# Kernel tuning notes

Measured on AMD Instinct MI355X. Metric: run time of the kernel, lower is better.

Reference implementation:

```python
import jax, jax.numpy as jnp
import numpy as np

D_MODEL = 1024
N_HEADS = 16
D_K = D_MODEL // N_HEADS
THETA = 10000.0


def _rope(x, token_positions):
    # x: [b, h, s, d_k]; interleaved RoPE (pairs at even/odd positions)
    half = D_K // 2
    inv_freq = 1.0 / (THETA ** (2.0 * jnp.arange(half, dtype=jnp.float32) / D_K))  # [half]
    angles = token_positions.astype(jnp.float32)[:, None] * inv_freq[None, :]      # [s, half]
    sin, cos = jnp.sin(angles), jnp.cos(angles)
    x_even = x[..., 0::2]
    x_odd = x[..., 1::2]
    out_even = cos * x_even - sin * x_odd
    out_odd = sin * x_even + cos * x_odd
    # interleave back: [..., half, 2] -> [..., d_k]
    return jnp.stack((out_even, out_odd), axis=-1).reshape(x.shape)


def setup_inputs() -> dict:
    key = jax.random.key(0)
    kx, kq, kk, kv, ko = jax.random.split(key, 5)
    b, s = 4, 2048
    std = (2.0 / (D_MODEL + D_MODEL)) ** 0.5
    return {
        "x": jax.random.normal(kx, (b, s, D_MODEL), dtype=jnp.float32),
        "Wq": jax.random.normal(kq, (D_MODEL, D_MODEL), dtype=jnp.float32) * std,
        "Wk": jax.random.normal(kk, (D_MODEL, D_MODEL), dtype=jnp.float32) * std,
        "Wv": jax.random.normal(kv, (D_MODEL, D_MODEL), dtype=jnp.float32) * std,
        "Wo": jax.random.normal(ko, (D_MODEL, D_MODEL), dtype=jnp.float32) * std,
        "token_positions": jnp.arange(s, dtype=jnp.int32),
    }


def reference(x, Wq, Wk, Wv, Wo, token_positions):
    b, s, _ = x.shape
    split = lambda t: t.reshape(b, s, N_HEADS, D_K).transpose(0, 2, 1, 3)  # b h s d
    q = split(x @ Wq.T)
    k = split(x @ Wk.T)
    v = split(x @ Wv.T)
    q = _rope(q, token_positions)
    k = _rope(k, token_positions)
    scores = jnp.einsum("bhnd,bhmd->bhnm", q, k) / jnp.sqrt(jnp.float32(D_K))
    causal = jnp.tril(jnp.ones((s, s), dtype=bool))
    scores = jnp.where(causal, scores, -jnp.inf)
    attn = jax.nn.softmax(scores, axis=-1)
    out = jnp.einsum("bhnm,bhmd->bhnd", attn, v)
    out = out.transpose(0, 2, 1, 3).reshape(b, s, D_MODEL)
    return out @ Wo.T
```

## Files before the change

kernel.cpp:

```cpp
#include <hip/hip_runtime.h>
#include <stdint.h>

typedef __attribute__((ext_vector_type(8))) __bf16 bf16x8;
typedef __attribute__((ext_vector_type(4))) float f32x4;
typedef __attribute__((ext_vector_type(16))) float f32x16;
typedef __attribute__((ext_vector_type(8))) unsigned short ushort8;

__device__ __forceinline__ unsigned short f2bf(float f){
  union { float f; unsigned int i; } v; v.f = f;
  unsigned int r = v.i + 0x7fffu + ((v.i >> 16) & 1u);
  return (unsigned short)(r >> 16);
}
__device__ __forceinline__ void gload16(const void* g, void* l){
  __builtin_amdgcn_global_load_lds((__attribute__((address_space(1))) void*)(g),
                                   (__attribute__((address_space(3))) void*)(l),
                                   16, 0, 0);
}
__device__ __forceinline__ unsigned int cvtpk(float lo, float hi){
  unsigned int r;
  asm("v_cvt_pk_bf16_f32 %0, %1, %2" : "=v"(r) : "v"(lo), "v"(hi));
  return r;
}
__device__ __forceinline__ bf16x8 ldsw(const char* tile, int row, int colb){
  return *(const bf16x8*)(tile + row*128 + (colb ^ ((row & 7) << 4)));
}

#define SEQ   2048
#define DM    1024
#define NH    16
#define DK    64
#define BATCH 4
#define MTOT  (BATCH*SEQ)
#define NX    (MTOT*DM)
#define NW    (DM*DM)

#define QSCALE 0.18033688011112f

__global__ __launch_bounds__(256) void k_tables(const int* __restrict__ pos,
                                                float* __restrict__ tab)
{
  const int idx = blockIdx.x * 256 + threadIdx.x;
  const int s = idx >> 5, i = idx & 31;
  const float inv = __expf(-0.28782313662425575f * (float)i);
  const float a = (float)pos[s] * inv;
  tab[2*idx]   = cosf(a);
  tab[2*idx+1] = sinf(a);
}

__global__ __launch_bounds__(256) void k_convert(
    const float* __restrict__ x,  const float* __restrict__ wq,
    const float* __restrict__ wk, const float* __restrict__ wv,
    const float* __restrict__ wo,
    unsigned short* __restrict__ xb, unsigned short* __restrict__ wb)
{
  const int tid = blockIdx.x * 256 + threadIdx.x;
  const long long e = (long long)tid * 8;
  const float* src; unsigned short* dst;
  if (e < NX) { src = x + e; dst = xb + e; }
  else {
    long long j = e - NX;
    int seg = (int)(j >> 20);
    long long off = j & 1048575;
    src = (seg==0?wq:seg==1?wk:seg==2?wv:wo) + off;
    dst = wb + (size_t)seg*NW + off;
  }
  const float4 a = *(const float4*)src;
  const float4 b = *(const float4*)(src + 4);
  uint4 o;
  o.x = (unsigned int)f2bf(a.x) | ((unsigned int)f2bf(a.y) << 16);
  o.y = (unsigned int)f2bf(a.z) | ((unsigned int)f2bf(a.w) << 16);
  o.z = (unsigned int)f2bf(b.x) | ((unsigned int)f2bf(b.y) << 16);
  o.w = (unsigned int)f2bf(b.z) | ((unsigned int)f2bf(b.w) << 16);
  *(uint4*)dst = o;
}

#define BK 32
#define NTK (DM/BK)

template<int MODE>
__global__ __launch_bounds__(512, 3) void k_gemm(
    const unsigned short* __restrict__ A,
    const unsigned short* __restrict__ Wb,
    unsigned short* __restrict__ D0,
    unsigned short* __restrict__ D1,
    unsigned short* __restrict__ D2,
    float* __restrict__ Dout,
    const float* __restrict__ tab)
{
  __shared__ __attribute__((aligned(16))) unsigned short As[2][256*BK];
  __shared__ __attribute__((aligned(16))) unsigned short Bs[2][128*BK];
  const int tid  = threadIdx.x;
  const int lane = tid & 63;
  const int w    = tid >> 6;
  const int wm = w >> 1, wn = w & 1;

  const int bid = blockIdx.x;
  const int tq  = bid >> 3;
  const int m0  = ((bid & 7)*4 + (tq & 3)) * 256;
  const int r   = tq >> 2;
  const int n0  = (MODE == 0 ? (r & 7) : r) * 128;
  const int z   = (MODE == 0) ? (r >> 3) : 0;

  const unsigned short* W = Wb + (size_t)z * NW;
  unsigned short* Dh = (MODE == 0) ? ((z == 0) ? D0 : (z == 1) ? D1 : D2) : nullptr;
  const bool vtr = (MODE == 0) && (z == 2);

  f32x4 acc[4][4];
  #pragma unroll
  for (int i = 0; i < 4; ++i)
    #pragma unroll
    for (int j = 0; j < 4; ++j)
      acc[i][j] = (f32x4)0.0f;

  auto stage = [&](int buf, int t){
    const int k0 = t * BK;
    #pragma unroll
    for (int cc = 0; cc < 2; ++cc){
      const int f = cc*512 + tid;
      const int row = f >> 2, kc = f & 3;
      const int kcs = kc ^ ((row >> 1) & 3);
      gload16(A + (size_t)(m0 + row)*DM + k0 + kcs*8,
              (char*)&As[buf][0] + (cc*512 + w*64)*16);
    }
    {
      const int row = tid >> 2, kc = tid & 3;
      const int kcs = kc ^ ((row >> 1) & 3);
      gload16(W + (size_t)(n0 + row)*DM + k0 + kcs*8,
              (char*)&Bs[buf][0] + (w*64)*16);
    }
  };

  stage(0, 0);
  __syncthreads();
  int cur = 0;
  for (int t = 0; t < NTK; ++t){
    if (t + 1 < NTK) stage(cur ^ 1, t + 1);
    const char* Ab_ = (const char*)&As[cur][0];
    const char* Bb_ = (const char*)&Bs[cur][0];
    bf16x8 af[4], bfr[4];
    #pragma unroll
    for (int i = 0; i < 4; ++i){
      const int rowA = wm*64 + i*16 + (lane & 15);
      const int rowB = wn*64 + i*16 + (lane & 15);
      af[i]  = *(const bf16x8*)(Ab_ + rowA*64 + ((((lane >> 4) ^ (rowA >> 1)) & 3) << 4));
      bfr[i] = *(const bf16x8*)(Bb_ + rowB*64 + ((((lane >> 4) ^ (rowB >> 1)) & 3) << 4));
    }
    #pragma unroll
    for (int i = 0; i < 4; ++i)
      #pragma unroll
      for (int j = 0; j < 4; ++j)
        acc[i][j] = __builtin_amdgcn_mfma_f32_16x16x32_bf16(af[i], bfr[j], acc[i][j], 0, 0, 0);
    __syncthreads();
    cur ^= 1;
  }

  if (MODE == 0 && !vtr){
    const float scale = (z == 0) ? QSCALE : 1.0f;
    #pragma unroll
    for (int i = 0; i < 4; ++i)
      #pragma unroll
      for (int j = 0; j < 4; ++j)
        #pragma unroll
        for (int rr = 0; rr < 4; ++rr){
          const int m = m0 + wm*64 + i*16 + ((lane >> 4) << 2) + rr;
          const int n = n0 + wn*64 + j*16 + (lane & 15);
          const float v  = acc[i][j][rr];
          const float vp = __shfl_xor(v, 1, 64);
          const int sp = m & 2047, d = n & 63;
          const float2 cs = ((const float2*)tab)[sp*32 + (d >> 1)];
          const float o = ((n & 1) ? (cs.y*vp + cs.x*v) : (cs.x*v - cs.y*vp)) * scale;
          const int b = m >> 11, hh = n >> 6;
          *(__bf16*)&Dh[((size_t)((b*NH + hh)*SEQ + sp))*DK + d] = (__bf16)o;
        }
  } else {
    #pragma unroll
    for (int i = 0; i < 4; ++i)
      #pragma unroll
      for (int j = 0; j < 4; ++j)
        #pragma unroll
        for (int rr = 0; rr < 4; ++rr){
          const int m = m0 + wm*64 + i*16 + ((lane >> 4) << 2) + rr;
          const int n = n0 + wn*64 + j*16 + (lane & 15);
          if (MODE == 0){
            const int b = m >> 11, sp = m & 2047, hh = n >> 6, d = n & 63;
            *(__bf16*)&Dh[(((size_t)(b*NH + hh))*DK + d)*SEQ + sp] = (__bf16)acc[i][j][rr];
          } else {
            Dout[(size_t)m * DM + n] = acc[i][j][rr];
          }
        }
  }
}

__global__ __launch_bounds__(512, 4) void k_attn(const unsigned short* __restrict__ Qh,
                                                 const unsigned short* __restrict__ Kh,
                                                 const unsigned short* __restrict__ Vt,
                                                 unsigned short* __restrict__ Ab)
{
  __shared__ uint4 ldsu[4096];
  char* base = (char*)ldsu;
  const int tid  = threadIdx.x;
  const int lane = tid & 63;
  const int w    = tid >> 6;
  const int ww   = w & 3;
  const int g    = w >> 2;
  const int tl   = tid & 255;
  const int l31  = lane & 31;
  const int hl   = lane >> 5;
  char* gb = base + g*32768;

  const int jj = blockIdx.x, bh = blockIdx.y;
  const unsigned short* Qb = Qh + (size_t)bh*(SEQ*DK);
  const unsigned short* Kb = Kh + (size_t)bh*(SEQ*DK);
  const unsigned short* Vb = Vt + (size_t)bh*(SEQ*DK);
  const int b = bh >> 4, hd = bh & 15;

  for (int pass = 0; pass < 2; ++pass){
    const int qt = pass ? jj : 15 - jj;
    const int q0 = qt * 128;
    const int qbase = q0 + ww*32;

    bf16x8 qf[4];
    #pragma unroll
    for (int t = 0; t < 4; ++t)
      qf[t] = *(const bf16x8*)(Qb + (size_t)(qbase + l31)*DK + t*16 + hl*8);

    f32x16 acc0 = (f32x16)0.0f, acc1 = (f32x16)0.0f;
    float lsum = 0.0f;

    const int nk = qt + 1;
    const int tbase = g * nk;
    const int wqmax = qbase + 31;

    auto stage = [&](int buf, int ktile){
      const int k0s = ktile * 64;
      char* Kd = gb + buf*16384;
      char* Vd = Kd + 8192;
      #pragma unroll
      for (int cc = 0; cc < 2; ++cc){
        const int f = cc*256 + tl;
        const int r = f >> 3, slot = f & 7;
        const int sw = ((slot ^ (r & 7)) << 3);
        gload16(Kb + (size_t)(k0s + r)*DK + sw, Kd + (cc*256 + ww*64)*16);
        gload16(Vb + (size_t)r*SEQ + k0s + sw, Vd + (cc*256 + ww*64)*16);
      }
    };

    if (pass) __syncthreads();
    stage(0, tbase);
    __syncthreads();
    int cur = 0;

    for (int kt = 0; kt < nk; ++kt){
      const int k0 = (tbase + kt) * 64;
      if (kt + 1 < nk) stage(cur ^ 1, tbase + kt + 1);
      if (k0 <= wqmax){
        const char* Ks = gb + cur*16384;
        const char* Vs = Ks + 8192;

        f32x16 sv0 = (f32x16)0.0f, sv1 = (f32x16)0.0f;
        __builtin_amdgcn_s_setprio(1);
        #pragma unroll
        for (int t = 0; t < 4; ++t){
          const int colb = t*32 + hl*16;
          const bf16x8 a0 = ldsw(Ks, l31, colb);
          const bf16x8 a1 = ldsw(Ks, 32 + l31, colb);
          sv0 = __builtin_amdgcn_mfma_f32_32x32x16_bf16(a0, qf[t], sv0, 0, 0, 0);
          sv1 = __builtin_amdgcn_mfma_f32_32x32x16_bf16(a1, qf[t], sv1, 0, 0, 0);
        }
        __builtin_amdgcn_s_setprio(0);

        if (k0 + 63 > qbase){
          const int q = qbase + l31;
          #pragma unroll
          for (int j = 0; j < 16; ++j){
            const int kv = k0 + (j&3) + 8*(j>>2) + 4*hl;
            if (kv > q)      sv0[j] = -1e30f;
            if (kv + 32 > q) sv1[j] = -1e30f;
          }
        }

        #pragma unroll
        for (int j = 0; j < 16; ++j){
          sv0[j] = exp2f(sv0[j]);
          sv1[j] = exp2f(sv1[j]);
        }
        float ts[8];
        #pragma unroll
        for (int j = 0; j < 8; ++j)
          ts[j] = (sv0[j] + sv0[j+8]) + (sv1[j] + sv1[j+8]);
        #pragma unroll
        for (int off = 4; off; off >>= 1)
          #pragma unroll
          for (int j = 0; j < off; ++j)
            ts[j] += ts[j+off];
        lsum += ts[0] + __shfl_xor(ts[0], 32, 64);

        __builtin_amdgcn_s_setprio(1);
        #pragma unroll
        for (int t = 0; t < 4; ++t){
          f32x16& s = (t < 2) ? sv0 : sv1;
          const int b0v = (t & 1) * 8;
          const unsigned int A0 = cvtpk(s[b0v+0], s[b0v+1]);
          const unsigned int A1 = cvtpk(s[b0v+2], s[b0v+3]);
          const unsigned int B0 = cvtpk(s[b0v+4], s[b0v+5]);
          const unsigned int B1 = cvtpk(s[b0v+6], s[b0v+7]);
          const unsigned int s0 = hl ? A0 : B0;
          const unsigned int s1 = hl ? A1 : B1;
          const unsigned int r0 = (unsigned int)__shfl_xor((int)s0, 32, 64);
          const unsigned int r1 = (unsigned int)__shfl_xor((int)s1, 32, 64);
          union { unsigned int u[4]; bf16x8 v; } f;
          f.u[0] = hl ? r0 : A0; f.u[1] = hl ? r1 : A1;
          f.u[2] = hl ? B0 : r0; f.u[3] = hl ? B1 : r1;
          const int colb = t*32 + hl*16;
          const bf16x8 v0 = ldsw(Vs, l31, colb);
          const bf16x8 v1 = ldsw(Vs, 32 + l31, colb);
          acc0 = __builtin_amdgcn_mfma_f32_32x32x16_bf16(v0, f.v, acc0, 0, 0, 0);
          acc1 = __builtin_amdgcn_mfma_f32_32x32x16_bf16(v1, f.v, acc1, 0, 0, 0);
        }
        __builtin_amdgcn_s_setprio(0);
      }
      __syncthreads();
      cur ^= 1;
    }

    if (g == 1){
      char* cw = base + ww*9216 + lane*144;
      #pragma unroll
      for (int q4 = 0; q4 < 4; ++q4){
        *(f32x4*)(cw + q4*16)      = (f32x4){acc0[4*q4], acc0[4*q4+1], acc0[4*q4+2], acc0[4*q4+3]};
        *(f32x4*)(cw + 64 + q4*16) = (f32x4){acc1[4*q4], acc1[4*q4+1], acc1[4*q4+2], acc1[4*q4+3]};
      }
      *(float*)(cw + 128) = lsum;
    }
    __syncthreads();
    if (g == 0){
      const char* cr = base + ww*9216 + lane*144;
      const float l1 = *(const float*)(cr + 128);
      const float linv = 1.0f / (lsum + l1);
      unsigned short* orow = Ab + ((size_t)(b*SEQ + qbase + l31))*DM + hd*DK;
      #pragma unroll
      for (int mt = 0; mt < 2; ++mt){
        #pragma unroll
        for (int g4 = 0; g4 < 4; ++g4){
          const f32x16& a = mt ? acc1 : acc0;
          const f32x4 o = *(const f32x4*)(cr + mt*64 + g4*16);
          const unsigned int u0 = cvtpk((a[4*g4+0] + o[0])*linv, (a[4*g4+1] + o[1])*linv);
          const unsigned int u1 = cvtpk((a[4*g4+2] + o[2])*linv, (a[4*g4+3] + o[3])*linv);
          *(unsigned long long*)(orow + mt*32 + g4*8 + hl*4) =
              (unsigned long long)u0 | ((unsigned long long)u1 << 32);
        }
      }
    }
  }
}

extern "C" void kernel_launch(void* const* d_in, const int* in_sizes, int n_in,
                              void* d_out, int out_size, void* d_ws, size_t ws_size,
                              hipStream_t stream)
{
  (void)in_sizes; (void)n_in; (void)out_size;
  const float* x  = (const float*)d_in[0];
  const float* wq = (const float*)d_in[1];
  const float* wk = (const float*)d_in[2];
  const float* wv = (const float*)d_in[3];
  const float* wo = (const float*)d_in[4];
  const int* pos  = (const int*)d_in[5];
  float* out = (float*)d_out;

  if (ws_size < 92800000u) return;
  char* ws = (char*)d_ws;
  unsigned short* xb = (unsigned short*)(ws);
  unsigned short* wb = (unsigned short*)(ws + 16777216);
  unsigned short* Qh = (unsigned short*)(ws + 25165824);
  unsigned short* Kh = (unsigned short*)(ws + 41943040);
  unsigned short* Vt = (unsigned short*)(ws + 75497472);
  float* tab         = (float*)(ws + 92274688);

  k_tables  <<<256, 256, 0, stream>>>(pos, tab);
  k_convert <<<6144, 256, 0, stream>>>(x, wq, wk, wv, wo, xb, wb);
  k_gemm<0> <<<768, 512, 0, stream>>>(xb, wb, Qh, Kh, Vt, nullptr, tab);
  k_attn    <<<dim3(8, 64), 512, 0, stream>>>(Qh, Kh, Vt, xb);
  k_gemm<1> <<<256, 512, 0, stream>>>(xb, wb + 3*NW, nullptr, nullptr,
                                      nullptr, out, nullptr);
}
```

Before: 189.5 us.

## Triple-buffer GEMM main loop with BK=64 and interleaved loads, barriers, setprio

Rewrites the GEMM main loop to use a K-tile of 64 with three LDS stages and prefetch two tiles ahead. Global-to-LDS loads are split into chunks and interleaved between MFMA phases, with explicit vmcnt/lgkmcnt waits and s_setprio around the MFMA groups. The aim is to halve the number of loop iterations and barriers per K and to hide global load latency better. In exchange LDS use rises to 144KB, occupancy drops to 2 blocks per CU, and correctness now depends on hand-counted waitcnt values.

```diff
diff --git a/kernel.cpp b/kernel.cpp
--- a/kernel.cpp
+++ b/kernel.cpp
@@ -74,11 +74,13 @@
   *(uint4*)dst = o;
 }
 
-#define BK 32
-#define NTK (DM/BK)
+#define BK64 64
+#define NT   (DM/BK64)
+#define ABUF 32768
+#define BSTRIDE 49152
 
 template<int MODE>
-__global__ __launch_bounds__(512, 3) void k_gemm(
+__global__ __launch_bounds__(512, 2) void k_gemm(
     const unsigned short* __restrict__ A,
     const unsigned short* __restrict__ Wb,
     unsigned short* __restrict__ D0,
@@ -87,8 +89,7 @@
     float* __restrict__ Dout,
     const float* __restrict__ tab)
 {
-  __shared__ __attribute__((aligned(16))) unsigned short As[2][256*BK];
-  __shared__ __attribute__((aligned(16))) unsigned short Bs[2][128*BK];
+  __shared__ __attribute__((aligned(16))) char lds_[3*BSTRIDE];
   const int tid  = threadIdx.x;
   const int lane = tid & 63;
   const int w    = tid >> 6;
@@ -112,46 +113,106 @@
     for (int j = 0; j < 4; ++j)
       acc[i][j] = (f32x4)0.0f;
 
-  auto stage = [&](int buf, int t){
-    const int k0 = t * BK;
-    #pragma unroll
-    for (int cc = 0; cc < 2; ++cc){
-      const int f = cc*512 + tid;
-      const int row = f >> 2, kc = f & 3;
-      const int kcs = kc ^ ((row >> 1) & 3);
-      gload16(A + (size_t)(m0 + row)*DM + k0 + kcs*8,
-              (char*)&As[buf][0] + (cc*512 + w*64)*16);
-    }
-    {
-      const int row = tid >> 2, kc = tid & 3;
-      const int kcs = kc ^ ((row >> 1) & 3);
-      gload16(W + (size_t)(n0 + row)*DM + k0 + kcs*8,
-              (char*)&Bs[buf][0] + (w*64)*16);
-    }
+  auto stA = [&](int buf, int t, int l){
+    const int k0 = t * BK64;
+    const int id = l*512 + tid;
+    const int row = id >> 3, c = id & 7;
+    gload16(A + (size_t)(m0 + row)*DM + k0 + ((c ^ (row & 7)) << 3),
+            lds_ + buf*BSTRIDE + id*16);
   };
-
-  stage(0, 0);
-  __syncthreads();
-  int cur = 0;
-  for (int t = 0; t < NTK; ++t){
-    if (t + 1 < NTK) stage(cur ^ 1, t + 1);
-    const char* Ab_ = (const char*)&As[cur][0];
-    const char* Bb_ = (const char*)&Bs[cur][0];
-    bf16x8 af[4], bfr[4];
-    #pragma unroll
-    for (int i = 0; i < 4; ++i){
-      const int rowA = wm*64 + i*16 + (lane & 15);
-      const int rowB = wn*64 + i*16 + (lane & 15);
-      af[i]  = *(const bf16x8*)(Ab_ + rowA*64 + ((((lane >> 4) ^ (rowA >> 1)) & 3) << 4));
-      bfr[i] = *(const bf16x8*)(Bb_ + rowB*64 + ((((lane >> 4) ^ (rowB >> 1)) & 3) << 4));
-    }
-    #pragma unroll
-    for (int i = 0; i < 4; ++i)
-      #pragma unroll
-      for (int j = 0; j < 4; ++j)
-        acc[i][j] = __builtin_amdgcn_mfma_f32_16x16x32_bf16(af[i], bfr[j], acc[i][j], 0, 0, 0);
-    __syncthreads();
-    cur ^= 1;
+  auto stB = [&](int buf, int t, int l){
+    const int k0 = t * BK64;
+    const int id = l*512 + tid;
+    const int row = id >> 3, c = id & 7;
+    gload16(W + (size_t)(n0 + row)*DM + k0 + ((c ^ (row & 7)) << 3),
+            lds_ + buf*BSTRIDE + ABUF + id*16);
+  };
+  auto ldA = [&](const char* Ab_, int i, int kk){
+    const int row = wm*64 + i*16 + (lane & 15);
+    const int c = (kk*4 + (lane >> 4)) ^ (row & 7);
+    return *(const bf16x8*)(Ab_ + row*128 + (c << 4));
+  };
+  auto ldB = [&](const char* Bb_, int j, int kk){
+    const int row = wn*64 + j*16 + (lane & 15);
+    const int c = (kk*4 + (lane >> 4)) ^ (row & 7);
+    return *(const bf16x8*)(Bb_ + row*128 + (c << 4));
+  };
+
+  #pragma unroll
+  for (int l = 0; l < 4; ++l) stA(0, 0, l);
+  stB(0, 0, 0); stB(0, 0, 1);
+  #pragma unroll
+  for (int l = 0; l < 4; ++l) stA(1, 1, l);
+  stB(1, 1, 0); stB(1, 1, 1);
+  asm volatile("s_waitcnt vmcnt(6)" ::: "memory");
+  __builtin_amdgcn_s_barrier();
+
+  int rb = 0, sb = 2;
+  for (int t = 0; t < NT; ++t){
+    const char* Ab_ = lds_ + rb*BSTRIDE;
+    const char* Bb_ = Ab_ + ABUF;
+    const bool st = (t + 2 < NT);
+    bf16x8 aF0, aF1, bF[4];
+
+    aF0 = ldA(Ab_, 0, 0); aF1 = ldA(Ab_, 1, 0);
+    bF[0] = ldB(Bb_, 0, 0); bF[1] = ldB(Bb_, 1, 0);
+    bF[2] = ldB(Bb_, 2, 0); bF[3] = ldB(Bb_, 3, 0);
+    if (st){ stA(sb, t+2, 0); stA(sb, t+2, 1); }
+    __builtin_amdgcn_s_barrier();
+    asm volatile("s_waitcnt lgkmcnt(0)" ::: "memory");
+    __builtin_amdgcn_s_setprio(1);
+    #pragma unroll
+    for (int j = 0; j < 4; ++j){
+      acc[0][j] = __builtin_amdgcn_mfma_f32_16x16x32_bf16(aF0, bF[j], acc[0][j], 0, 0, 0);
+      acc[1][j] = __builtin_amdgcn_mfma_f32_16x16x32_bf16(aF1, bF[j], acc[1][j], 0, 0, 0);
+    }
+    __builtin_amdgcn_s_setprio(0);
+    __builtin_amdgcn_s_barrier();
+
+    aF0 = ldA(Ab_, 2, 0); aF1 = ldA(Ab_, 3, 0);
+    if (st){ stA(sb, t+2, 2); stA(sb, t+2, 3); }
+    __builtin_amdgcn_s_barrier();
+    asm volatile("s_waitcnt lgkmcnt(0)" ::: "memory");
+    __builtin_amdgcn_s_setprio(1);
+    #pragma unroll
+    for (int j = 0; j < 4; ++j){
+      acc[2][j] = __builtin_amdgcn_mfma_f32_16x16x32_bf16(aF0, bF[j], acc[2][j], 0, 0, 0);
+      acc[3][j] = __builtin_amdgcn_mfma_f32_16x16x32_bf16(aF1, bF[j], acc[3][j], 0, 0, 0);
+    }
+    __builtin_amdgcn_s_setprio(0);
+    __builtin_amdgcn_s_barrier();
+
+    aF0 = ldA(Ab_, 0, 1); aF1 = ldA(Ab_, 1, 1);
+    bF[0] = ldB(Bb_, 0, 1); bF[1] = ldB(Bb_, 1, 1);
+    bF[2] = ldB(Bb_, 2, 1); bF[3] = ldB(Bb_, 3, 1);
+    if (st){ stB(sb, t+2, 0); stB(sb, t+2, 1); }
+    __builtin_amdgcn_s_barrier();
+    asm volatile("s_waitcnt lgkmcnt(0)" ::: "memory");
+    __builtin_amdgcn_s_setprio(1);
+    #pragma unroll
+    for (int j = 0; j < 4; ++j){
+      acc[0][j] = __builtin_amdgcn_mfma_f32_16x16x32_bf16(aF0, bF[j], acc[0][j], 0, 0, 0);
+      acc[1][j] = __builtin_amdgcn_mfma_f32_16x16x32_bf16(aF1, bF[j], acc[1][j], 0, 0, 0);
+    }
+    __builtin_amdgcn_s_setprio(0);
+    __builtin_amdgcn_s_barrier();
+
+    aF0 = ldA(Ab_, 2, 1); aF1 = ldA(Ab_, 3, 1);
+    __builtin_amdgcn_s_barrier();
+    asm volatile("s_waitcnt lgkmcnt(0)" ::: "memory");
+    __builtin_amdgcn_s_setprio(1);
+    #pragma unroll
+    for (int j = 0; j < 4; ++j){
+      acc[2][j] = __builtin_amdgcn_mfma_f32_16x16x32_bf16(aF0, bF[j], acc[2][j], 0, 0, 0);
+      acc[3][j] = __builtin_amdgcn_mfma_f32_16x16x32_bf16(aF1, bF[j], acc[3][j], 0, 0, 0);
+    }
+    __builtin_amdgcn_s_setprio(0);
+    if (t < NT-2)       asm volatile("s_waitcnt vmcnt(6)" ::: "memory");
+    else if (t == NT-2) asm volatile("s_waitcnt vmcnt(0)" ::: "memory");
+    if (t < NT-1) __builtin_amdgcn_s_barrier();
+
+    rb = (rb == 2) ? 0 : rb + 1;
+    sb = (sb == 2) ? 0 : sb + 1;
   }
 
   if (MODE == 0 && !vtr){
```

Result: faster. 177.3 us (-6.4%).
